# Optimization experiments

Measured on AMD Instinct MI355X. Metric: run time of the kernel, lower is better.

Reference implementation:

```python
import jax, jax.numpy as jnp
import numpy as np

N_TOKENS = 65536
D_MODEL = 256
N_EXPERTS = 32
NEG_INF = -1e38


def setup_inputs() -> dict:
    key = jax.random.key(0)
    k_x, k_wg, k_wn, k_we, k_noise = jax.random.split(key, 5)
    x = jax.random.normal(k_x, (N_TOKENS, D_MODEL), dtype=jnp.float32)
    # gating and noise projections: Linear(d_model -> n_experts), no bias
    Wg = jax.random.normal(k_wg, (D_MODEL, N_EXPERTS), dtype=jnp.float32) * 0.02
    Wnoise = jax.random.normal(k_wn, (D_MODEL, N_EXPERTS), dtype=jnp.float32) * 0.02
    # experts: one Linear(d_model -> d_model) per expert
    We = jax.random.normal(k_we, (N_EXPERTS, D_MODEL, D_MODEL), dtype=jnp.float32) * 0.02
    be = jnp.zeros((N_EXPERTS, D_MODEL), dtype=jnp.float32)
    # torch.randn(nexperts): one shared noise vector broadcast over tokens
    noise_vec = jax.random.normal(k_noise, (N_EXPERTS,), dtype=jnp.float32)
    return {"x": x, "Wg": Wg, "Wnoise": Wnoise, "We": We, "be": be,
            "noise_vec": noise_vec, "top_k": 2}


def reference(x, Wg, Wnoise, We, be, noise_vec, top_k):
    # Eq. (4): H = x Wg + randn * softplus(x Wnoise)   -> [N, E]
    g = x @ Wg
    H = g + noise_vec[None, :] * jax.nn.softplus(x @ Wnoise)
    # Keep top_k largest per row (original masks the bottom E-k with -Inf)
    vals, idx = jax.lax.top_k(H, top_k)                      # [N, k]
    rows = jnp.arange(H.shape[0])[:, None]
    keep = jnp.full_like(H, NEG_INF).at[rows, idx].set(vals)  # [N, E]
    G = jax.nn.softmax(keep, axis=1)                          # [N, E], k nonzeros
    # Dense all-expert compute (as in the original): E_out [N, E, D]
    E_out = jnp.einsum('nd,edh->neh', x, We) + be[None, :, :]
    # Weighted sum over experts
    return jnp.einsum('ne,neh->nh', G, E_out)                 # [N, D]
```

## Files before the change

### kernel.cpp

```cpp
#include <hip/hip_runtime.h>

#define NT 65536
#define DM 256
#define NE 32

typedef __attribute__((ext_vector_type(8))) short v8bf;
typedef __attribute__((ext_vector_type(4))) float v4f;

#define C_RISKY 0
#define C_TC1 1
#define C_TC2 2
#define C_HIST1 8
#define C_HIST2 40
#define C_CUR1 72
#define C_CUR2 104

__device__ __forceinline__ unsigned short f2bf(float f) {
  union { float f; unsigned u; } v; v.f = f;
  unsigned r = v.u + 0x7FFFu + ((v.u >> 16) & 1u);
  return (unsigned short)(r >> 16);
}

__global__ __launch_bounds__(256) void prep_w(const float* __restrict__ Wg,
                                              const float* __restrict__ Wn,
                                              float* __restrict__ wgn,
                                              unsigned short* __restrict__ wgnb) {
  int i = blockIdx.x * 256 + threadIdx.x;
  if (i < 256 * 64) {
    int k = i >> 6, c = i & 63;
    float v = (c < 32) ? Wg[k * 32 + c] : Wn[k * 32 + (c - 32)];
    wgn[i] = v;
    wgnb[c * 256 + k] = f2bf(v);
  }
}

__global__ __launch_bounds__(256) void prep_wet(const float* __restrict__ We,
                                                unsigned short* __restrict__ WeT) {
  __shared__ float t[32][33];
  int e = blockIdx.x;
  int d0 = (blockIdx.y >> 3) * 32, h0 = (blockIdx.y & 7) * 32;
  int tx = threadIdx.x & 31, ty = threadIdx.x >> 5;
  const float* src = We + ((size_t)e * 256 + d0) * 256 + h0;
#pragma unroll
  for (int r = 0; r < 4; ++r) t[ty + r * 8][tx] = src[(size_t)(ty + r * 8) * 256 + tx];
  __syncthreads();
  unsigned short* dst = WeT + ((size_t)e * 256 + h0) * 256 + d0;
#pragma unroll
  for (int r = 0; r < 4; ++r) dst[(size_t)(ty + r * 8) * 256 + tx] = f2bf(t[tx][ty + r * 8]);
}

__global__ __launch_bounds__(256) void gate_kernel(const float* __restrict__ x,
                                                   const unsigned short* __restrict__ wgnb,
                                                   const float* __restrict__ nvec,
                                                   int4* __restrict__ records,
                                                   int* __restrict__ risky,
                                                   int* __restrict__ ctrl,
                                                   unsigned short* __restrict__ xbf,
                                                   int use_xbf) {
  __shared__ __align__(16) union {
    struct { short Al[128 * 72]; short Bl[64 * 72]; } t;
    float H[128 * 67];
  } sm;
  __shared__ float nvs[32];
  __shared__ int lh[64];
  int tid = threadIdx.x;
  if (tid < 64) lh[tid] = 0;
  if (tid < 32) nvs[tid] = nvec[tid];
  int t0 = blockIdx.x * 128;
  int lane = tid & 63, wid = tid >> 6;
  int wm = wid * 32;
  int lm = lane & 15, lk = (lane >> 4) * 8;
  v4f acc[2][4];
  v4f zero = {0.f, 0.f, 0.f, 0.f};
#pragma unroll
  for (int mi = 0; mi < 2; ++mi)
#pragma unroll
    for (int ni = 0; ni < 4; ++ni) acc[mi][ni] = zero;
  for (int k0 = 0; k0 < 256; k0 += 64) {
    __syncthreads();
#pragma unroll
    for (int j = 0; j < 4; ++j) {
      int idx = tid + 256 * j;
      int row = idx >> 3, kc = idx & 7;
      const float4* s = (const float4*)(x + ((size_t)(t0 + row) * 256 + k0 + kc * 8));
      float4 a = s[0], b = s[1];
      union { v8bf v; unsigned short u[8]; uint4 q; } p;
      p.u[0] = f2bf(a.x); p.u[1] = f2bf(a.y); p.u[2] = f2bf(a.z); p.u[3] = f2bf(a.w);
      p.u[4] = f2bf(b.x); p.u[5] = f2bf(b.y); p.u[6] = f2bf(b.z); p.u[7] = f2bf(b.w);
      *(v8bf*)(sm.t.Al + row * 72 + kc * 8) = p.v;
      if (use_xbf) *(uint4*)(xbf + ((size_t)(t0 + row) * 256 + k0 + kc * 8)) = p.q;
    }
#pragma unroll
    for (int j = 0; j < 2; ++j) {
      int idx = tid + 256 * j;
      int col = idx >> 3, kc = idx & 7;
      uint4 w = *(const uint4*)(wgnb + ((size_t)col * 256 + k0 + kc * 8));
      *(uint4*)(sm.t.Bl + col * 72 + kc * 8) = w;
    }
    __syncthreads();
#pragma unroll
    for (int ks = 0; ks < 64; ks += 32) {
      v8bf af[2], bfr[4];
#pragma unroll
      for (int mi = 0; mi < 2; ++mi)
        af[mi] = *(const v8bf*)(sm.t.Al + (wm + mi * 16 + lm) * 72 + ks + lk);
#pragma unroll
      for (int ni = 0; ni < 4; ++ni)
        bfr[ni] = *(const v8bf*)(sm.t.Bl + (ni * 16 + lm) * 72 + ks + lk);
#pragma unroll
      for (int mi = 0; mi < 2; ++mi)
#pragma unroll
        for (int ni = 0; ni < 4; ++ni)
          acc[mi][ni] = __builtin_amdgcn_mfma_f32_16x16x32_bf16(af[mi], bfr[ni], acc[mi][ni], 0, 0, 0);
    }
  }
  __syncthreads();
  int cg = lane & 15, rg = lane >> 4;
#pragma unroll
  for (int mi = 0; mi < 2; ++mi)
#pragma unroll
    for (int r = 0; r < 4; ++r) {
      int row = wm + mi * 16 + rg * 4 + r;
#pragma unroll
      for (int ni = 0; ni < 4; ++ni) sm.H[row * 67 + ni * 16 + cg] = acc[mi][ni][r];
    }
  __syncthreads();
  if (tid < 128) {
    int t = t0 + tid;
    float v1 = -3e38f, v2 = -3e38f, v3 = -3e38f;
    int i1 = 0, i2 = 0;
#pragma unroll 4
    for (int e = 0; e < 32; ++e) {
      float g = sm.H[tid * 67 + e];
      float n = sm.H[tid * 67 + 32 + e];
      float sp = fmaxf(n, 0.f) + log1pf(expf(-fabsf(n)));
      float he = fmaf(nvs[e], sp, g);
      if (he > v1) { v3 = v2; v2 = v1; i2 = i1; v1 = he; i1 = e; }
      else if (he > v2) { v3 = v2; v2 = he; i2 = e; }
      else if (he > v3) v3 = he;
    }
    float w1v = 1.f / (1.f + expf(v2 - v1));
    float w2v = 1.f / (1.f + expf(v1 - v2));
    records[t] = make_int4(i1, i2, __float_as_int(w1v), __float_as_int(w2v));
    atomicAdd(&lh[i1], 1);
    atomicAdd(&lh[32 + i2], 1);
    if (v2 - v3 < 2e-2f) {
      int p = atomicAdd(&ctrl[C_RISKY], 1);
      risky[p] = t;
    }
  }
  __syncthreads();
  if (tid < 32) atomicAdd(&ctrl[C_HIST1 + tid], lh[tid]);
  else if (tid < 64) atomicAdd(&ctrl[C_HIST2 + (tid - 32)], lh[tid]);
}

__global__ __launch_bounds__(256) void fixup_kernel(const float* __restrict__ x,
                                                    const float* __restrict__ wgn,
                                                    const float* __restrict__ nvec,
                                                    int4* __restrict__ records,
                                                    const int* __restrict__ risky,
                                                    int* __restrict__ ctrl) {
  int cnt = ctrl[C_RISKY];
  int lane = threadIdx.x & 63, wid = threadIdx.x >> 6;
  for (int r = blockIdx.x * 4 + wid; r < cnt; r += gridDim.x * 4) {
    int t = __builtin_amdgcn_readfirstlane(risky[r]);
    const float* xr = x + (size_t)t * 256;
    double a0 = 0.0, a1 = 0.0, a2 = 0.0, a3 = 0.0;
    for (int k = 0; k < 256; k += 4) {
      float4 xv = *(const float4*)(xr + k);
      a0 = fma((double)xv.x, (double)wgn[(k + 0) * 64 + lane], a0);
      a1 = fma((double)xv.y, (double)wgn[(k + 1) * 64 + lane], a1);
      a2 = fma((double)xv.z, (double)wgn[(k + 2) * 64 + lane], a2);
      a3 = fma((double)xv.w, (double)wgn[(k + 3) * 64 + lane], a3);
    }
    double acc = (a0 + a1) + (a2 + a3);
    double sv = __shfl(acc, lane + 32);
    double H;
    if (lane < 32) {
      double sp = fmax(sv, 0.0) + log1p(exp(-fabs(sv)));
      H = acc + (double)nvec[lane] * sp;
    } else
      H = -1e300;
    double v = H; int idx = lane;
#pragma unroll
    for (int off = 32; off >= 1; off >>= 1) {
      double ov = __shfl_xor(v, off); int oi = __shfl_xor(idx, off);
      if (ov > v || (ov == v && oi < idx)) { v = ov; idx = oi; }
    }
    int i1 = idx; double v1 = v;
    v = (lane == i1) ? -1e300 : H; idx = lane;
#pragma unroll
    for (int off = 32; off >= 1; off >>= 1) {
      double ov = __shfl_xor(v, off); int oi = __shfl_xor(idx, off);
      if (ov > v || (ov == v && oi < idx)) { v = ov; idx = oi; }
    }
    int i2 = idx; double v2 = v;
    if (lane == 0) {
      float w1v = (float)(1.0 / (1.0 + exp(v2 - v1)));
      float w2v = (float)(1.0 / (1.0 + exp(v1 - v2)));
      int4 old = records[t];
      if (old.x != i1) { atomicSub(&ctrl[C_HIST1 + old.x], 1); atomicAdd(&ctrl[C_HIST1 + i1], 1); }
      if (old.y != i2) { atomicSub(&ctrl[C_HIST2 + old.y], 1); atomicAdd(&ctrl[C_HIST2 + i2], 1); }
      records[t] = make_int4(i1, i2, __float_as_int(w1v), __float_as_int(w2v));
    }
  }
}

__global__ __launch_bounds__(64) void scan_kernel(int* __restrict__ ctrl,
                                                  int4* __restrict__ table1,
                                                  int4* __restrict__ table2) {
  __shared__ int so1[32], so2[32], tp1[32], tp2[32];
  int tid = threadIdx.x;
  if (tid == 0) {
    int o = 0, tp = 0;
    for (int e = 0; e < 32; ++e) {
      so1[e] = o; tp1[e] = tp;
      int c = ctrl[C_HIST1 + e];
      o += c; tp += (c + 127) >> 7;
    }
    ctrl[C_TC1] = tp;
    o = 0; tp = 0;
    for (int e = 0; e < 32; ++e) {
      so2[e] = o; tp2[e] = tp;
      int c = ctrl[C_HIST2 + e];
      o += c; tp += (c + 127) >> 7;
    }
    ctrl[C_TC2] = tp;
  }
  __syncthreads();
  if (tid < 32) {
    int e = tid;
    ctrl[C_CUR1 + e] = so1[e];
    int c = ctrl[C_HIST1 + e];
    int nt = (c + 127) >> 7;
    for (int m = 0; m < nt; ++m)
      table1[tp1[e] + m] = make_int4(e, so1[e] + m * 128, min(128, c - m * 128), 0);
  } else if (tid < 64) {
    int e = tid - 32;
    ctrl[C_CUR2 + e] = so2[e];
    int c = ctrl[C_HIST2 + e];
    int nt = (c + 127) >> 7;
    for (int m = 0; m < nt; ++m)
      table2[tp2[e] + m] = make_int4(e, so2[e] + m * 128, min(128, c - m * 128), 0);
  }
}

__global__ __launch_bounds__(256) void scatter_kernel(const int4* __restrict__ records,
                                                      int* __restrict__ ctrl,
                                                      int* __restrict__ perm1, float* __restrict__ pw1,
                                                      int* __restrict__ perm2, float* __restrict__ pw2) {
  __shared__ int lh1[32], lh2[32], b1[32], b2[32];
  int tid = threadIdx.x;
  if (tid < 32) { lh1[tid] = 0; lh2[tid] = 0; }
  __syncthreads();
  int t = blockIdx.x * 256 + tid;
  int4 rec = records[t];
  int r1 = atomicAdd(&lh1[rec.x], 1);
  int r2 = atomicAdd(&lh2[rec.y], 1);
  __syncthreads();
  if (tid < 32) {
    b1[tid] = atomicAdd(&ctrl[C_CUR1 + tid], lh1[tid]);
    b2[tid] = atomicAdd(&ctrl[C_CUR2 + tid], lh2[tid]);
  }
  __syncthreads();
  int s1 = b1[rec.x] + r1; perm1[s1] = t; pw1[s1] = __int_as_float(rec.z);
  int s2 = b2[rec.y] + r2; perm2[s2] = t; pw2[s2] = __int_as_float(rec.w);
}

__global__ __launch_bounds__(256) void expert_kernel(const float* __restrict__ x,
                                                     const unsigned short* __restrict__ xbf,
                                                     int use_xbf,
                                                     const unsigned short* __restrict__ WeT,
                                                     const float* __restrict__ be,
                                                     const int* __restrict__ perm,
                                                     const float* __restrict__ pw,
                                                     const int4* __restrict__ table,
                                                     const int* __restrict__ tcp,
                                                     float* __restrict__ out,
                                                     int accumulate) {
  int nt = *tcp;
  if (blockIdx.x >= nt) return;
  int4 ent = table[blockIdx.x];
  int e = ent.x, sbase = ent.y, rows = ent.z;
  int n0 = blockIdx.y * 128;
  __shared__ __align__(16) short Al[128 * 72];
  __shared__ __align__(16) short Bl[128 * 72];
  __shared__ int toks[128];
  int tid = threadIdx.x;
  if (tid < 128) toks[tid] = perm[sbase + min(tid, rows - 1)];
  v4f acc[4][4];
  v4f zero = {0.f, 0.f, 0.f, 0.f};
#pragma unroll
  for (int mi = 0; mi < 4; ++mi)
#pragma unroll
    for (int ni = 0; ni < 4; ++ni) acc[mi][ni] = zero;
  int lane = tid & 63, wid = tid >> 6;
  int wm = (wid & 1) * 64, wn = (wid >> 1) * 64;
  int lm = lane & 15, lk = (lane >> 4) * 8;
  for (int k0 = 0; k0 < 256; k0 += 64) {
    __syncthreads();
#pragma unroll
    for (int j = 0; j < 4; ++j) {
      int idx = tid + 256 * j;
      int row = idx >> 3, kc = idx & 7;
      if (use_xbf) {
        uint4 v = *(const uint4*)(xbf + ((size_t)toks[row] * 256 + k0 + kc * 8));
        *(uint4*)(Al + row * 72 + kc * 8) = v;
      } else {
        const float4* s = (const float4*)(x + ((size_t)toks[row] * 256 + k0 + kc * 8));
        float4 a = s[0], b = s[1];
        union { v8bf v; unsigned short u[8]; } p;
        p.u[0] = f2bf(a.x); p.u[1] = f2bf(a.y); p.u[2] = f2bf(a.z); p.u[3] = f2bf(a.w);
        p.u[4] = f2bf(b.x); p.u[5] = f2bf(b.y); p.u[6] = f2bf(b.z); p.u[7] = f2bf(b.w);
        *(v8bf*)(Al + row * 72 + kc * 8) = p.v;
      }
      uint4 w = *(const uint4*)(WeT + (((size_t)e * 256 + n0 + row) * 256 + k0 + kc * 8));
      *(uint4*)(Bl + row * 72 + kc * 8) = w;
    }
    __syncthreads();
#pragma unroll
    for (int ks = 0; ks < 64; ks += 32) {
      v8bf af[4], bfr[4];
#pragma unroll
      for (int mi = 0; mi < 4; ++mi)
        af[mi] = *(const v8bf*)(Al + (wm + mi * 16 + lm) * 72 + ks + lk);
#pragma unroll
      for (int ni = 0; ni < 4; ++ni)
        bfr[ni] = *(const v8bf*)(Bl + (wn + ni * 16 + lm) * 72 + ks + lk);
#pragma unroll
      for (int mi = 0; mi < 4; ++mi)
#pragma unroll
        for (int ni = 0; ni < 4; ++ni)
          acc[mi][ni] = __builtin_amdgcn_mfma_f32_16x16x32_bf16(af[mi], bfr[ni], acc[mi][ni], 0, 0, 0);
    }
  }
  int cg = lane & 15, rg = lane >> 4;
#pragma unroll
  for (int mi = 0; mi < 4; ++mi) {
#pragma unroll
    for (int r = 0; r < 4; ++r) {
      int srow = wm + mi * 16 + rg * 4 + r;
      if (srow < rows) {
        int slot = sbase + srow;
        int tok = perm[slot];
        float w = pw[slot];
        size_t ob = (size_t)tok * 256;
#pragma unroll
        for (int ni = 0; ni < 4; ++ni) {
          int c = n0 + wn + ni * 16 + cg;
          float v = acc[mi][ni][r] * w + w * be[e * 256 + c];
          if (accumulate) out[ob + c] += v;
          else out[ob + c] = v;
        }
      }
    }
  }
}

extern "C" void kernel_launch(void* const* d_in, const int* in_sizes, int n_in,
                              void* d_out, int out_size, void* d_ws, size_t ws_size,
                              hipStream_t stream) {
  const float* x = (const float*)d_in[0];
  const float* Wg = (const float*)d_in[1];
  const float* Wn = (const float*)d_in[2];
  const float* We = (const float*)d_in[3];
  const float* be = (const float*)d_in[4];
  const float* nvec = (const float*)d_in[5];
  float* out = (float*)d_out;
  char* ws = (char*)d_ws;
  size_t off = 0;
  auto alloc = [&](size_t bytes) -> void* {
    void* p = ws + off;
    off = (off + bytes + 255) & ~(size_t)255;
    return p;
  };
  int* ctrl = (int*)alloc(4096);
  int4* records = (int4*)alloc((size_t)NT * 16);
  int* risky = (int*)alloc((size_t)NT * 4);
  int* perm1 = (int*)alloc((size_t)NT * 4);
  float* pw1 = (float*)alloc((size_t)NT * 4);
  int* perm2 = (int*)alloc((size_t)NT * 4);
  float* pw2 = (float*)alloc((size_t)NT * 4);
  int4* table1 = (int4*)alloc(1024 * 16);
  int4* table2 = (int4*)alloc(1024 * 16);
  float* wgn = (float*)alloc(256 * 64 * 4);
  unsigned short* wgnb = (unsigned short*)alloc(64 * 256 * 2);
  unsigned short* WeT = (unsigned short*)alloc((size_t)NE * 256 * 256 * 2);
  unsigned short* xbf = nullptr;
  int use_xbf = 0;
  if (off + (size_t)NT * 256 * 2 <= ws_size) {
    xbf = (unsigned short*)alloc((size_t)NT * 256 * 2);
    use_xbf = 1;
  }

  hipMemsetAsync(ctrl, 0, 4096, stream);
  prep_w<<<64, 256, 0, stream>>>(Wg, Wn, wgn, wgnb);
  prep_wet<<<dim3(32, 64), 256, 0, stream>>>(We, WeT);
  gate_kernel<<<NT / 128, 256, 0, stream>>>(x, wgnb, nvec, records, risky, ctrl, xbf, use_xbf);
  fixup_kernel<<<256, 256, 0, stream>>>(x, wgn, nvec, records, risky, ctrl);
  scan_kernel<<<1, 64, 0, stream>>>(ctrl, table1, table2);
  scatter_kernel<<<NT / 256, 256, 0, stream>>>(records, ctrl, perm1, pw1, perm2, pw2);
  expert_kernel<<<dim3(544, 2), 256, 0, stream>>>(x, xbf, use_xbf, WeT, be, perm1, pw1, table1,
                                                  ctrl + C_TC1, out, 0);
  expert_kernel<<<dim3(544, 2), 256, 0, stream>>>(x, xbf, use_xbf, WeT, be, perm2, pw2, table2,
                                                  ctrl + C_TC2, out, 1);
}
```

Before: 389.4 us.

## Stage GEMM tiles via direct global-to-LDS loads with XOR-swizzled layout

Moves the fp32-to-bf16 conversion of x into a separate convert kernel. The gate and expert kernels then load bf16 tiles straight into LDS with global_load_lds, bypassing registers. The padded 72-stride LDS layout is replaced by an unpadded 64-stride one with an XOR swizzle to avoid bank conflicts on fragment reads. This cuts VGPR traffic and staging instructions, at the cost of an extra kernel pass that reads x and writes xbf before gating.

```diff
diff --git a/kernel.cpp b/kernel.cpp
--- a/kernel.cpp
+++ b/kernel.cpp
@@ -19,6 +19,22 @@
   union { float f; unsigned u; } v; v.f = f;
   unsigned r = v.u + 0x7FFFu + ((v.u >> 16) & 1u);
   return (unsigned short)(r >> 16);
+}
+
+#define GLOAD_LDS16(g, l)                                                     \
+  __builtin_amdgcn_global_load_lds(                                           \
+      (const __attribute__((address_space(1))) unsigned int*)(g),             \
+      (__attribute__((address_space(3))) unsigned int*)(l), 16, 0, 0)
+
+__global__ __launch_bounds__(256) void convert_kernel(const float* __restrict__ x,
+                                                      unsigned short* __restrict__ xbf) {
+  size_t i = (size_t)blockIdx.x * 256 + threadIdx.x;
+  const float4* s = (const float4*)x + i * 2;
+  float4 a = s[0], b = s[1];
+  union { v8bf v; unsigned short u[8]; uint4 q; } p;
+  p.u[0] = f2bf(a.x); p.u[1] = f2bf(a.y); p.u[2] = f2bf(a.z); p.u[3] = f2bf(a.w);
+  p.u[4] = f2bf(b.x); p.u[5] = f2bf(b.y); p.u[6] = f2bf(b.z); p.u[7] = f2bf(b.w);
+  *(uint4*)(xbf + i * 8) = p.q;
 }
 
 __global__ __launch_bounds__(256) void prep_w(const float* __restrict__ Wg,
@@ -50,15 +66,15 @@
 }
 
 __global__ __launch_bounds__(256) void gate_kernel(const float* __restrict__ x,
+                                                   const unsigned short* __restrict__ xbf,
+                                                   int use_xbf,
                                                    const unsigned short* __restrict__ wgnb,
                                                    const float* __restrict__ nvec,
                                                    int4* __restrict__ records,
                                                    int* __restrict__ risky,
-                                                   int* __restrict__ ctrl,
-                                                   unsigned short* __restrict__ xbf,
-                                                   int use_xbf) {
+                                                   int* __restrict__ ctrl) {
   __shared__ __align__(16) union {
-    struct { short Al[128 * 72]; short Bl[64 * 72]; } t;
+    struct { short Al[128 * 64]; short Bl[64 * 64]; } t;
     float H[128 * 67];
   } sm;
   __shared__ float nvs[32];
@@ -69,7 +85,9 @@
   int t0 = blockIdx.x * 128;
   int lane = tid & 63, wid = tid >> 6;
   int wm = wid * 32;
-  int lm = lane & 15, lk = (lane >> 4) * 8;
+  int lm = lane & 15, lk8 = (lane >> 4) * 8;
+  int r0 = tid >> 3, kc = tid & 7;
+  int kcs = kc ^ (r0 & 7);
   v4f acc[2][4];
   v4f zero = {0.f, 0.f, 0.f, 0.f};
 #pragma unroll
@@ -78,35 +96,47 @@
     for (int ni = 0; ni < 4; ++ni) acc[mi][ni] = zero;
   for (int k0 = 0; k0 < 256; k0 += 64) {
     __syncthreads();
-#pragma unroll
-    for (int j = 0; j < 4; ++j) {
-      int idx = tid + 256 * j;
-      int row = idx >> 3, kc = idx & 7;
-      const float4* s = (const float4*)(x + ((size_t)(t0 + row) * 256 + k0 + kc * 8));
-      float4 a = s[0], b = s[1];
-      union { v8bf v; unsigned short u[8]; uint4 q; } p;
-      p.u[0] = f2bf(a.x); p.u[1] = f2bf(a.y); p.u[2] = f2bf(a.z); p.u[3] = f2bf(a.w);
-      p.u[4] = f2bf(b.x); p.u[5] = f2bf(b.y); p.u[6] = f2bf(b.z); p.u[7] = f2bf(b.w);
-      *(v8bf*)(sm.t.Al + row * 72 + kc * 8) = p.v;
-      if (use_xbf) *(uint4*)(xbf + ((size_t)(t0 + row) * 256 + k0 + kc * 8)) = p.q;
-    }
-#pragma unroll
-    for (int j = 0; j < 2; ++j) {
-      int idx = tid + 256 * j;
-      int col = idx >> 3, kc = idx & 7;
-      uint4 w = *(const uint4*)(wgnb + ((size_t)col * 256 + k0 + kc * 8));
-      *(uint4*)(sm.t.Bl + col * 72 + kc * 8) = w;
+    if (use_xbf) {
+#pragma unroll
+      for (int j = 0; j < 4; ++j)
+        GLOAD_LDS16(xbf + ((size_t)(t0 + r0 + 32 * j) * 256 + k0 + kcs * 8),
+                    sm.t.Al + (size_t)(256 * j + (tid & 192)) * 8);
+#pragma unroll
+      for (int j = 0; j < 2; ++j)
+        GLOAD_LDS16(wgnb + ((size_t)(r0 + 32 * j) * 256 + k0 + kcs * 8),
+                    sm.t.Bl + (size_t)(256 * j + (tid & 192)) * 8);
+    } else {
+#pragma unroll
+      for (int j = 0; j < 4; ++j) {
+        const float4* s = (const float4*)(x + ((size_t)(t0 + r0 + 32 * j) * 256 + k0 + kcs * 8));
+        float4 a = s[0], b = s[1];
+        union { v8bf v; unsigned short u[8]; } p;
+        p.u[0] = f2bf(a.x); p.u[1] = f2bf(a.y); p.u[2] = f2bf(a.z); p.u[3] = f2bf(a.w);
+        p.u[4] = f2bf(b.x); p.u[5] = f2bf(b.y); p.u[6] = f2bf(b.z); p.u[7] = f2bf(b.w);
+        *(v8bf*)(sm.t.Al + (size_t)(tid + 256 * j) * 8) = p.v;
+      }
+#pragma unroll
+      for (int j = 0; j < 2; ++j) {
+        uint4 w = *(const uint4*)(wgnb + ((size_t)(r0 + 32 * j) * 256 + k0 + kcs * 8));
+        *(uint4*)(sm.t.Bl + (size_t)(tid + 256 * j) * 8) = w;
+      }
     }
     __syncthreads();
 #pragma unroll
     for (int ks = 0; ks < 64; ks += 32) {
+      int c = (ks + lk8) >> 3;
+      int cs = c ^ (lm & 7);
       v8bf af[2], bfr[4];
 #pragma unroll
-      for (int mi = 0; mi < 2; ++mi)
-        af[mi] = *(const v8bf*)(sm.t.Al + (wm + mi * 16 + lm) * 72 + ks + lk);
-#pragma unroll
-      for (int ni = 0; ni < 4; ++ni)
-        bfr[ni] = *(const v8bf*)(sm.t.Bl + (ni * 16 + lm) * 72 + ks + lk);
+      for (int mi = 0; mi < 2; ++mi) {
+        int r = wm + mi * 16 + lm;
+        af[mi] = *(const v8bf*)(sm.t.Al + (size_t)(r * 8 + cs) * 8);
+      }
+#pragma unroll
+      for (int ni = 0; ni < 4; ++ni) {
+        int cr = ni * 16 + lm;
+        bfr[ni] = *(const v8bf*)(sm.t.Bl + (size_t)(cr * 8 + cs) * 8);
+      }
 #pragma unroll
       for (int mi = 0; mi < 2; ++mi)
 #pragma unroll
@@ -283,50 +313,66 @@
   int4 ent = table[blockIdx.x];
   int e = ent.x, sbase = ent.y, rows = ent.z;
   int n0 = blockIdx.y * 128;
-  __shared__ __align__(16) short Al[128 * 72];
-  __shared__ __align__(16) short Bl[128 * 72];
-  __shared__ int toks[128];
+  __shared__ __align__(16) short Al[128 * 64];
+  __shared__ __align__(16) short Bl[128 * 64];
   int tid = threadIdx.x;
-  if (tid < 128) toks[tid] = perm[sbase + min(tid, rows - 1)];
+  int lane = tid & 63, wid = tid >> 6;
+  int wm = (wid & 1) * 64, wn = (wid >> 1) * 64;
+  int lm = lane & 15, lk8 = (lane >> 4) * 8;
+  int r0 = tid >> 3, kc = tid & 7;
+  int kcs = kc ^ (r0 & 7);
+  int tok[4];
+#pragma unroll
+  for (int j = 0; j < 4; ++j) tok[j] = perm[sbase + min(r0 + 32 * j, rows - 1)];
   v4f acc[4][4];
   v4f zero = {0.f, 0.f, 0.f, 0.f};
 #pragma unroll
   for (int mi = 0; mi < 4; ++mi)
 #pragma unroll
     for (int ni = 0; ni < 4; ++ni) acc[mi][ni] = zero;
-  int lane = tid & 63, wid = tid >> 6;
-  int wm = (wid & 1) * 64, wn = (wid >> 1) * 64;
-  int lm = lane & 15, lk = (lane >> 4) * 8;
   for (int k0 = 0; k0 < 256; k0 += 64) {
     __syncthreads();
-#pragma unroll
-    for (int j = 0; j < 4; ++j) {
-      int idx = tid + 256 * j;
-      int row = idx >> 3, kc = idx & 7;
-      if (use_xbf) {
-        uint4 v = *(const uint4*)(xbf + ((size_t)toks[row] * 256 + k0 + kc * 8));
-        *(uint4*)(Al + row * 72 + kc * 8) = v;
-      } else {
-        const float4* s = (const float4*)(x + ((size_t)toks[row] * 256 + k0 + kc * 8));
+    if (use_xbf) {
+#pragma unroll
+      for (int j = 0; j < 4; ++j)
+        GLOAD_LDS16(xbf + ((size_t)tok[j] * 256 + k0 + kcs * 8),
+                    Al + (size_t)(256 * j + (tid & 192)) * 8);
+#pragma unroll
+      for (int j = 0; j < 4; ++j)
+        GLOAD_LDS16(WeT + (((size_t)e * 256 + n0 + r0 + 32 * j) * 256 + k0 + kcs * 8),
+                    Bl + (size_t)(256 * j + (tid & 192)) * 8);
+    } else {
+#pragma unroll
+      for (int j = 0; j < 4; ++j) {
+        const float4* s = (const float4*)(x + ((size_t)tok[j] * 256 + k0 + kcs * 8));
         float4 a = s[0], b = s[1];
         union { v8bf v; unsigned short u[8]; } p;
         p.u[0] = f2bf(a.x); p.u[1] = f2bf(a.y); p.u[2] = f2bf(a.z); p.u[3] = f2bf(a.w);
         p.u[4] = f2bf(b.x); p.u[5] = f2bf(b.y); p.u[6] = f2bf(b.z); p.u[7] = f2bf(b.w);
-        *(v8bf*)(Al + row * 72 + kc * 8) = p.v;
-      }
-      uint4 w = *(const uint4*)(WeT + (((size_t)e * 256 + n0 + row) * 256 + k0 + kc * 8));
-      *(uint4*)(Bl + row * 72 + kc * 8) = w;
+        *(v8bf*)(Al + (size_t)(tid + 256 * j) * 8) = p.v;
+      }
+#pragma unroll
+      for (int j = 0; j < 4; ++j) {
+        uint4 w = *(const uint4*)(WeT + (((size_t)e * 256 + n0 + r0 + 32 * j) * 256 + k0 + kcs * 8));
+        *(uint4*)(Bl + (size_t)(tid + 256 * j) * 8) = w;
+      }
     }
     __syncthreads();
 #pragma unroll
     for (int ks = 0; ks < 64; ks += 32) {
+      int c = (ks + lk8) >> 3;
+      int cs = c ^ (lm & 7);
       v8bf af[4], bfr[4];
 #pragma unroll
-      for (int mi = 0; mi < 4; ++mi)
-        af[mi] = *(const v8bf*)(Al + (wm + mi * 16 + lm) * 72 + ks + lk);
-#pragma unroll
-      for (int ni = 0; ni < 4; ++ni)
-        bfr[ni] = *(const v8bf*)(Bl + (wn + ni * 16 + lm) * 72 + ks + lk);
+      for (int mi = 0; mi < 4; ++mi) {
+        int r = wm + mi * 16 + lm;
+        af[mi] = *(const v8bf*)(Al + (size_t)(r * 8 + cs) * 8);
+      }
+#pragma unroll
+      for (int ni = 0; ni < 4; ++ni) {
+        int cr = wn + ni * 16 + lm;
+        bfr[ni] = *(const v8bf*)(Bl + (size_t)(cr * 8 + cs) * 8);
+      }
 #pragma unroll
       for (int mi = 0; mi < 4; ++mi)
 #pragma unroll
@@ -342,9 +388,9 @@
       int srow = wm + mi * 16 + rg * 4 + r;
       if (srow < rows) {
         int slot = sbase + srow;
-        int tok = perm[slot];
+        int tokr = perm[slot];
         float w = pw[slot];
-        size_t ob = (size_t)tok * 256;
+        size_t ob = (size_t)tokr * 256;
 #pragma unroll
         for (int ni = 0; ni < 4; ++ni) {
           int c = n0 + wn + ni * 16 + cg;
@@ -396,7 +442,8 @@
   hipMemsetAsync(ctrl, 0, 4096, stream);
   prep_w<<<64, 256, 0, stream>>>(Wg, Wn, wgn, wgnb);
   prep_wet<<<dim3(32, 64), 256, 0, stream>>>(We, WeT);
-  gate_kernel<<<NT / 128, 256, 0, stream>>>(x, wgnb, nvec, records, risky, ctrl, xbf, use_xbf);
+  if (use_xbf) convert_kernel<<<NT * DM / 8 / 256, 256, 0, stream>>>(x, xbf);
+  gate_kernel<<<NT / 128, 256, 0, stream>>>(x, xbf, use_xbf, wgnb, nvec, records, risky, ctrl);
   fixup_kernel<<<256, 256, 0, stream>>>(x, wgn, nvec, records, risky, ctrl);
   scan_kernel<<<1, 64, 0, stream>>>(ctrl, table1, table2);
   scatter_kernel<<<NT / 256, 256, 0, stream>>>(records, ctrl, perm1, pw1, perm2, pw2);
```

Result: slower. 406.6 us (+4.4%).
